# Optimization experiments

Hardware: AMD Instinct MI355X
Metric: run time of the kernel (lower is better)

Reference implementation:

```python
import jax, jax.numpy as jnp
from jax import lax
import numpy as np

B, CIN, H, W = 32, 3, 128, 128
HID = 256          # hidden_dim == embedding_dim
K = 512            # num_embeddings
CC = 0.25          # commitment_cost
RR = 16            # SE reduction ratio


def setup_inputs() -> dict:
    key = jax.random.key(0)
    ks = iter(jax.random.split(key, 40))
    def n(shape, s=0.05):
        return jax.random.normal(next(ks), shape, jnp.float32) * s
    inp = {"x": jax.random.normal(next(ks), (B, CIN, H, W), jnp.float32)}
    inp.update(
        ec1_w=n((HID, CIN, 4, 4)), ec1_b=n((HID,)),
        ec2_w=n((HID, HID, 2, 2)), ec2_b=n((HID,)),
        se1_w1=n((HID // RR, HID)), se1_b1=n((HID // RR,)), se1_w2=n((HID, HID // RR)), se1_b2=n((HID,)), sa1_w=n((1, 2, 7, 7)),
        se2_w1=n((HID // RR, HID)), se2_b1=n((HID // RR,)), se2_w2=n((HID, HID // RR)), se2_b2=n((HID,)), sa2_w=n((1, 2, 7, 7)),
        codebook=jax.random.uniform(next(ks), (K, HID), jnp.float32, -1.0 / K, 1.0 / K),
        dt1_w=n((HID, HID, 2, 2)), dt1_b=n((HID,)),
        dt2_w=n((HID, CIN, 4, 4)), dt2_b=n((CIN,)),
        dse_w1=n((HID // RR, HID)), dse_b1=n((HID // RR,)), dse_w2=n((HID, HID // RR)), dse_b2=n((HID,)), dsa_w=n((2, 1, 7, 7)),
    )
    return inp


def conv(x, w, b, stride, pad=0):
    y = lax.conv_general_dilated(x, w, (stride, stride), [(pad, pad), (pad, pad)],
                                 dimension_numbers=('NCHW', 'OIHW', 'NCHW'))
    return y if b is None else y + b[None, :, None, None]


def convt(x, w, b, stride, pad=0):
    # torch ConvTranspose2d(weight [Cin, Cout, kh, kw]) == conv with flipped kernel,
    # lhs dilated by stride, padding k-1-pad
    k = w.shape[2]
    p = k - 1 - pad
    y = lax.conv_general_dilated(x, jnp.flip(w, (2, 3)), (1, 1), [(p, p), (p, p)],
                                 lhs_dilation=(stride, stride),
                                 dimension_numbers=('NCHW', 'IOHW', 'NCHW'))
    return y if b is None else y + b[None, :, None, None]


def se(x, w1, b1, w2, b2):
    s = jnp.mean(x, (2, 3))                                   # [B, C] global avg pool
    g = jax.nn.sigmoid(jax.nn.relu(s @ w1.T + b1) @ w2.T + b2)
    return x * g[:, :, None, None]


def cbam(x, w1, b1, w2, b2, sw, transpose=False):
    out = se(x, w1, b1, w2, b2)
    cat = jnp.concatenate([jnp.mean(out, 1, keepdims=True), jnp.max(out, 1, keepdims=True)], 1)
    s = convt(cat, sw, None, 1, 3) if transpose else conv(cat, sw, None, 1, 3)
    out = out * jax.nn.sigmoid(s)
    return x * out  # note: original CBAM.forward multiplies by x again


def vq(z, cb):
    D = cb.shape[1]
    flat = z.reshape(-1, D)  # faithful to torch reshape(-1, embedding_dim) on NCHW
    # squared euclidean distances (argmin identical to cdist argmin)
    d2 = jnp.sum(flat * flat, 1, keepdims=True) - 2.0 * (flat @ cb.T) + jnp.sum(cb * cb, 1)
    idx = jnp.argmin(d2, 1)
    q = cb[idx].reshape(z.shape)  # == one_hot(idx) @ cb, without materializing one-hot
    e_loss = jnp.mean((lax.stop_gradient(q) - z) ** 2)
    q_loss = jnp.mean((q - lax.stop_gradient(z)) ** 2)
    loss = q_loss + CC * e_loss
    q_st = z + lax.stop_gradient(q - z)
    p = jnp.zeros((cb.shape[0],), z.dtype).at[idx].add(1.0) / flat.shape[0]
    perplexity = jnp.exp(-jnp.sum(p * jnp.log(p + 1e-10)))
    return loss, q_st, perplexity


def reference(x, ec1_w, ec1_b, ec2_w, ec2_b,
              se1_w1, se1_b1, se1_w2, se1_b2, sa1_w,
              se2_w1, se2_b1, se2_w2, se2_b2, sa2_w,
              codebook, dt1_w, dt1_b, dt2_w, dt2_b,
              dse_w1, dse_b1, dse_w2, dse_b2, dsa_w):
    # encoder
    h = cbam(jax.nn.relu(conv(x, ec1_w, ec1_b, 2)), se1_w1, se1_b1, se1_w2, se1_b2, sa1_w)
    z = cbam(jax.nn.relu(conv(h, ec2_w, ec2_b, 1)), se2_w1, se2_b1, se2_w2, se2_b2, sa2_w)
    # vector quantization
    loss, q, perplexity = vq(z, codebook)
    # decoder
    d = cbam(jax.nn.relu(convt(q, dt1_w, dt1_b, 1)), dse_w1, dse_b1, dse_w2, dse_b2, dsa_w, transpose=True)
    x_recon = convt(d, dt2_w, dt2_b, 2)
    return x_recon, loss, perplexity
```

## Files before the change

kernel.cpp:

```cpp
#include <hip/hip_runtime.h>
#include <math.h>

#define NB 32
#define HID 256
#define HW1 (63*63)
#define HW2 (62*62)
#define T63 ((size_t)NB*HID*HW1)
#define T62 ((size_t)NB*HID*HW2)
#define NROWS 123008
#define KCB 512
#define GATHER_BLOCKS 1024

typedef __attribute__((ext_vector_type(8))) short short8;
typedef __attribute__((ext_vector_type(4))) float f32x4;
typedef __attribute__((ext_vector_type(4))) unsigned short us4;

__device__ __forceinline__ unsigned short f2bf(float f) {
    union { float f; unsigned int u; } v; v.f = f;
    unsigned int u = v.u;
    return (unsigned short)((u + 0x7FFFu + ((u >> 16) & 1u)) >> 16);
}
__device__ __forceinline__ float bf2f(unsigned short u) {
    union { unsigned int i; float f; } v; v.i = ((unsigned int)u) << 16;
    return v.f;
}

__global__ __launch_bounds__(256) void zero_small(float* __restrict__ sse, int* __restrict__ counts) {
    if (threadIdx.x == 0) sse[0] = 0.f;
    for (int i = threadIdx.x; i < KCB; i += 256) counts[i] = 0;
}
__global__ __launch_bounds__(256) void zero_pooled(float* __restrict__ pooled) {
    pooled[blockIdx.x*256 + threadIdx.x] = 0.f;
}

__global__ __launch_bounds__(256) void prepack_c1(
    const float* __restrict__ w, unsigned short* __restrict__ pack) {
    int t = blockIdx.x*256 + threadIdx.x;
    if (t >= 16384) return;
    int j = t & 7, lk = (t >> 3) & 3, co = (t >> 5) & 255, kc = t >> 13;
    int k = kc*32 + lk*8 + j;
    pack[t] = (k < 48) ? f2bf(w[co*48 + k]) : (unsigned short)0;
}

__global__ __launch_bounds__(256) void conv1_mfma(
    const float* __restrict__ x, const unsigned short* __restrict__ apack,
    const float* __restrict__ bias, unsigned short* __restrict__ X0) {
    __shared__ float xs[3][18][18];
    __shared__ __align__(16) unsigned short Bm[64*72];
    int b = blockIdx.y, t = blockIdx.x;
    int oh0 = (t >> 3)*8, ow0 = (t & 7)*8;
    int ih0 = oh0*2, iw0 = ow0*2;
    const float* xb = x + (size_t)b*3*128*128;
    for (int i = threadIdx.x; i < 972; i += 256) {
        int c = i / 324, rem = i - c*324, r = rem / 18, cl = rem - r*18;
        int ih = ih0 + r, iw = iw0 + cl;
        xs[c][r][cl] = (ih < 128 && iw < 128) ? xb[((size_t)c*128 + ih)*128 + iw] : 0.f;
    }
    __syncthreads();
    for (int i = threadIdx.x; i < 2048; i += 256) {
        int px = i >> 5, kp = (i & 31)*2;
        int ph = px >> 3, pw = px & 7;
        unsigned int pk = 0;
        #pragma unroll
        for (int u = 0; u < 2; ++u) {
            int k = kp + u;
            float v = 0.f;
            if (k < 48) {
                int c = k >> 4, k2 = k & 15, kh = k2 >> 2, kw = k2 & 3;
                v = xs[c][ph*2+kh][pw*2+kw];
            }
            pk |= ((unsigned int)f2bf(v)) << (16*u);
        }
        *(unsigned int*)&Bm[px*72 + kp] = pk;
    }
    __syncthreads();

    int w = threadIdx.x >> 6, l = threadIdx.x & 63;
    int lr = l & 15, lk = l >> 4;
    f32x4 acc[4][4];
    #pragma unroll
    for (int i = 0; i < 4; ++i)
        #pragma unroll
        for (int j = 0; j < 4; ++j) acc[i][j] = (f32x4){0.f,0.f,0.f,0.f};

    #pragma unroll
    for (int kc = 0; kc < 2; ++kc) {
        short8 bf[4];
        #pragma unroll
        for (int pxf = 0; pxf < 4; ++pxf)
            bf[pxf] = *(const short8*)&Bm[(pxf*16+lr)*72 + kc*32 + lk*8];
        #pragma unroll
        for (int cof = 0; cof < 4; ++cof) {
            int co = w*64 + cof*16 + lr;
            short8 af = *(const short8*)(apack + (((size_t)kc*256 + co)*4 + (size_t)lk)*8);
            acc[cof][0] = __builtin_amdgcn_mfma_f32_16x16x32_bf16(af, bf[0], acc[cof][0], 0, 0, 0);
            acc[cof][1] = __builtin_amdgcn_mfma_f32_16x16x32_bf16(af, bf[1], acc[cof][1], 0, 0, 0);
            acc[cof][2] = __builtin_amdgcn_mfma_f32_16x16x32_bf16(af, bf[2], acc[cof][2], 0, 0, 0);
            acc[cof][3] = __builtin_amdgcn_mfma_f32_16x16x32_bf16(af, bf[3], acc[cof][3], 0, 0, 0);
        }
    }
    #pragma unroll
    for (int cof = 0; cof < 4; ++cof) {
        int cob = w*64 + cof*16 + lk*4;
        float4 bz = *(const float4*)&bias[cob];
        #pragma unroll
        for (int pxf = 0; pxf < 4; ++pxf) {
            int px = pxf*16 + lr;
            int oh = oh0 + (px >> 3), ow = ow0 + (px & 7);
            if (oh < 63 && ow < 63) {
                f32x4 a = acc[cof][pxf];
                us4 pk = { f2bf(fmaxf(a.x + bz.x, 0.f)), f2bf(fmaxf(a.y + bz.y, 0.f)),
                           f2bf(fmaxf(a.z + bz.z, 0.f)), f2bf(fmaxf(a.w + bz.w, 0.f)) };
                *(us4*)(X0 + ((size_t)b*HW1 + (size_t)oh*63 + ow)*256 + cob) = pk;
            }
        }
    }
}

__global__ __launch_bounds__(256) void gap_nhwc(
    const unsigned short* __restrict__ X, float* __restrict__ pooled,
    int HW, float inv) {
    int b = blockIdx.y;
    int px0 = blockIdx.x * 512;
    int o = threadIdx.x & 31, pg = threadIdx.x >> 5;
    const unsigned short* xb = X + (size_t)b*HW*256 + o*8;
    float acc[8];
    #pragma unroll
    for (int j = 0; j < 8; ++j) acc[j] = 0.f;
    for (int i = 0; i < 64; ++i) {
        int px = px0 + pg + i*8;
        if (px < HW) {
            short8 v = *(const short8*)(xb + (size_t)px*256);
            #pragma unroll
            for (int j = 0; j < 8; ++j) acc[j] += bf2f((unsigned short)v[j]);
        }
    }
    __shared__ float pool2[8][256];
    #pragma unroll
    for (int j = 0; j < 8; ++j) pool2[pg][o*8+j] = acc[j];
    __syncthreads();
    float s = 0.f;
    #pragma unroll
    for (int p = 0; p < 8; ++p) s += pool2[p][threadIdx.x];
    atomicAdd(pooled + b*256 + threadIdx.x, s * inv);
}

__global__ __launch_bounds__(256) void gap_z(
    const unsigned short* __restrict__ Z, float* __restrict__ pooled, int HW) {
    int bc = blockIdx.x;
    const unsigned int* p = (const unsigned int*)(Z + (size_t)bc*HW);
    int n2 = HW >> 1;
    float s = 0.f;
    for (int i = threadIdx.x; i < n2; i += 256) {
        unsigned int v = p[i];
        s += bf2f((unsigned short)(v & 0xffff)) + bf2f((unsigned short)(v >> 16));
    }
    __shared__ float lds[4];
    for (int off = 32; off; off >>= 1) s += __shfl_down(s, off, 64);
    if ((threadIdx.x & 63) == 0) lds[threadIdx.x >> 6] = s;
    __syncthreads();
    if (threadIdx.x == 0) pooled[bc] = (lds[0]+lds[1]+lds[2]+lds[3]) / (float)HW;
}

__global__ __launch_bounds__(256) void se_mlp(
    const float* __restrict__ pooled, const float* __restrict__ w1,
    const float* __restrict__ b1, const float* __restrict__ w2,
    const float* __restrict__ b2, float* __restrict__ g) {
    int b = blockIdx.x;
    __shared__ float ps[256], hs[16];
    ps[threadIdx.x] = pooled[b*256 + threadIdx.x];
    __syncthreads();
    if (threadIdx.x < 16) {
        float a = b1[threadIdx.x];
        const float* wr = w1 + threadIdx.x*256;
        for (int k = 0; k < 256; ++k) a = fmaf(ps[k], wr[k], a);
        hs[threadIdx.x] = fmaxf(a, 0.f);
    }
    __syncthreads();
    float a = b2[threadIdx.x];
    const float* wr = w2 + threadIdx.x*16;
    #pragma unroll
    for (int j = 0; j < 16; ++j) a = fmaf(hs[j], wr[j], a);
    g[b*256 + threadIdx.x] = 1.f / (1.f + expf(-a));
}

__global__ __launch_bounds__(256) void chanpool_nhwc(
    const unsigned short* __restrict__ X, const float* __restrict__ g,
    float* __restrict__ am, int HW) {
    int b = blockIdx.y;
    __shared__ float gs[256];
    gs[threadIdx.x] = g[b*256 + threadIdx.x];
    __syncthreads();
    int p = blockIdx.x*256 + threadIdx.x;
    if (p >= HW) return;
    const unsigned short* xp = X + ((size_t)b*HW + p)*256;
    float s = 0.f, mx = -3.0e38f;
    for (int o = 0; o < 32; ++o) {
        short8 v = *(const short8*)(xp + o*8);
        #pragma unroll
        for (int j = 0; j < 8; ++j) {
            float f = bf2f((unsigned short)v[j]) * gs[o*8+j];
            s += f; mx = fmaxf(mx, f);
        }
    }
    am[((size_t)b*2)*HW + p]   = s * (1.f/256.f);
    am[((size_t)b*2+1)*HW + p] = mx;
}

__global__ __launch_bounds__(256) void chanpool_z(
    const unsigned short* __restrict__ Z, const float* __restrict__ g,
    float* __restrict__ am, int HW) {
    int b = blockIdx.y;
    __shared__ float gs[256];
    gs[threadIdx.x] = g[b*256 + threadIdx.x];
    __syncthreads();
    int p = blockIdx.x*256 + threadIdx.x;
    if (p >= HW) return;
    const unsigned short* xb = Z + (size_t)b*256*HW + p;
    float s = 0.f, mx = -3.0e38f;
    for (int c = 0; c < 256; ++c) {
        float v = bf2f(xb[(size_t)c*HW]) * gs[c];
        s += v; mx = fmaxf(mx, v);
    }
    am[((size_t)b*2)*HW + p]   = s * (1.f/256.f);
    am[((size_t)b*2+1)*HW + p] = mx;
}

__global__ __launch_bounds__(256) void spatial_conv(
    const float* __restrict__ am, const float* __restrict__ sw,
    float* __restrict__ ss, int H, int W, int transpose) {
    int b = blockIdx.y;
    int p = blockIdx.x*256 + threadIdx.x;
    __shared__ float ws[98];
    if (threadIdx.x < 98) {
        int c = threadIdx.x / 49, k = threadIdx.x % 49;
        int kh = k / 7, kw = k % 7;
        ws[threadIdx.x] = transpose ? sw[c*49 + (6-kh)*7 + (6-kw)]
                                    : sw[c*49 + kh*7 + kw];
    }
    __syncthreads();
    if (p >= H*W) return;
    int oh = p / W, ow = p % W;
    float acc = 0.f;
    #pragma unroll
    for (int c = 0; c < 2; ++c) {
        const float* ab = am + ((size_t)b*2 + c)*H*W;
        for (int kh = 0; kh < 7; ++kh) {
            int ih = oh + kh - 3;
            if (ih < 0 || ih >= H) continue;
            for (int kw = 0; kw < 7; ++kw) {
                int iw = ow + kw - 3;
                if (iw < 0 || iw >= W) continue;
                acc = fmaf(ab[(size_t)ih*W + iw], ws[c*49 + kh*7 + kw], acc);
            }
        }
    }
    ss[(size_t)b*H*W + p] = 1.f / (1.f + expf(-acc));
}

__global__ __launch_bounds__(256) void cbam_z(
    unsigned short* Z, const float* __restrict__ g,
    const float* __restrict__ ss, int HW) {
    int b = blockIdx.y;
    int e2 = blockIdx.x*256 + threadIdx.x;
    if (e2 >= 128*HW) return;
    size_t e = (size_t)e2*2;
    int c = (int)(e / HW), p = (int)(e % HW);
    float gc = g[b*256 + c];
    float s0 = ss[(size_t)b*HW + p];
    float s1 = ss[(size_t)b*HW + p + 1];
    unsigned int* px = (unsigned int*)(Z + (size_t)b*256*HW + e);
    unsigned int v = *px;
    float f0 = bf2f((unsigned short)(v & 0xffff));
    float f1 = bf2f((unsigned short)(v >> 16));
    f0 = f0*f0*gc*s0;
    f1 = f1*f1*gc*s1;
    *px = (unsigned int)f2bf(f0) | ((unsigned int)f2bf(f1) << 16);
}

__global__ __launch_bounds__(256) void to_nhwc_bf16(
    const unsigned short* __restrict__ Z, unsigned short* __restrict__ X, int HW) {
    int b = blockIdx.y;
    int p = blockIdx.x*256 + threadIdx.x;
    bool valid = p < HW;
    const unsigned short* inb = Z + (size_t)b*256*HW + p;
    unsigned short* dst = X + ((size_t)b*HW + p)*256;
    #pragma unroll
    for (int ch = 0; ch < 4; ++ch) {
        unsigned short buf[64];
        #pragma unroll
        for (int j = 0; j < 64; ++j)
            buf[j] = valid ? inb[(size_t)(ch*64 + j)*HW] : (unsigned short)0;
        if (valid) {
            #pragma unroll
            for (int j2 = 0; j2 < 8; ++j2)
                *(short8*)(dst + ch*64 + j2*8) = *(const short8*)&buf[j2*8];
        }
    }
}

__global__ __launch_bounds__(256) void prepack_w(
    const float* __restrict__ w, unsigned short* __restrict__ pack, int transpose_flip) {
    int t = blockIdx.x*256 + threadIdx.x;
    int j = t & 7, koct = (t >> 3) & 3, co = (t >> 5) & 255, tap = (t >> 13) & 3, cc = t >> 15;
    int ci = cc*32 + koct*8 + j;
    int kh = tap >> 1, kw = tap & 1;
    float v;
    if (transpose_flip) v = w[((size_t)ci*256 + co)*4 + (1-kh)*2 + (1-kw)];
    else                v = w[((size_t)co*256 + ci)*4 + kh*2 + kw];
    pack[t] = f2bf(v);
}

__global__ __launch_bounds__(256) void prepack_dt2b(
    const float* __restrict__ w, unsigned short* __restrict__ pk) {
    int t = blockIdx.x*256 + threadIdx.x;
    int jj = t & 7, lk = (t >> 3) & 3, co = (t >> 5) & 15, j = (t >> 9) & 3, cc = (t >> 11) & 7, p = t >> 14;
    int ci = cc*32 + lk*8 + jj;
    int kh0 = p >> 1, kw0 = p & 1;
    const int dj[4] = {0, 2, 8, 10};
    float v = 0.f;
    if (co < 3) v = w[(size_t)ci*48 + co*16 + kh0*4 + kw0 + dj[j]];
    pk[t] = f2bf(v);
}

template <int MODE>
__global__ __launch_bounds__(256) void convk2_mfma_nhwc(
    const unsigned short* __restrict__ Xin, const unsigned short* __restrict__ apack,
    const float* __restrict__ bias, const float* __restrict__ gvec,
    const float* __restrict__ ssm, unsigned short* __restrict__ outZ,
    unsigned short* __restrict__ outU,
    int inH, int inW, int outH, int outW, int pad) {
    __shared__ __align__(16) unsigned short Sh[MODE ? 16896 : 13600];
    __shared__ float gs[256];
    unsigned short* Ir0 = Sh;
    unsigned short* Ir1 = Sh + 6800;
    int b = blockIdx.y;
    int raw = blockIdx.x;
    int xcd = raw & 7, jj = raw >> 3;
    int t = (xcd + 8*(jj >> 2))*4 + (jj & 3);
    int oh0 = (t >> 2) * 4, ow0 = (t & 3) * 16;
    int w = threadIdx.x >> 6, l = threadIdx.x & 63;
    int lr = l & 15, lk = l >> 4;
    const unsigned short* src = Xin + (size_t)b*inH*inW*256;
    const float* ssb = (MODE == 0) ? (ssm + (size_t)b*inH*inW) : (const float*)0;
    if (MODE == 0) {
        gs[threadIdx.x] = gvec[b*256 + threadIdx.x];
        __syncthreads();
    }

    f32x4 acc[4][4];
    #pragma unroll
    for (int i = 0; i < 4; ++i)
        #pragma unroll
        for (int j = 0; j < 4; ++j) acc[i][j] = (f32x4){0.f,0.f,0.f,0.f};

    auto STAGE = [&](int cc, int bufi) {
        unsigned short* Ib = bufi ? Ir1 : Ir0;
        #pragma unroll
        for (int pass = 0; pass < 3; ++pass) {
            int u = pass*256 + threadIdx.x;
            if (u < 680) {
                int sub = (u >= 340) ? 1 : 0;
                int uu = u - sub*340;
                int sp = uu >> 2, q = uu & 3;
                int r = (sp*241) >> 12, c = sp - r*17;
                int gh = oh0 + r - pad, gw = ow0 + c - pad;
                short8 v = (short8){0,0,0,0,0,0,0,0};
                bool valid = (gh >= 0) && (gh < inH) && (gw >= 0) && (gw < inW);
                if (valid)
                    v = *(const short8*)(src + ((size_t)gh*inW + gw)*256 + (cc+sub)*32 + q*8);
                if (MODE == 0) {
                    if (valid) {
                        float sv = ssb[(size_t)gh*inW + gw];
                        int c0 = (cc+sub)*32 + q*8;
                        unsigned int pk[4];
                        #pragma unroll
                        for (int j = 0; j < 4; ++j) {
                            float f0 = bf2f((unsigned short)v[2*j]);
                            float f1 = bf2f((unsigned short)v[2*j+1]);
                            f0 = f0*f0*gs[c0+2*j]*sv;
                            f1 = f1*f1*gs[c0+2*j+1]*sv;
                            pk[j] = (unsigned int)f2bf(f0) | ((unsigned int)f2bf(f1) << 16);
                        }
                        v = *(const short8*)pk;
                    }
                }
                *(short8*)&Ib[sub*3400 + sp*40 + q*8] = v;
            }
        }
    };

    STAGE(0, 0);
    for (int cc = 0; cc < 8; cc += 2) {
        __syncthreads();
        if (cc < 6) STAGE(cc+2, ((cc >> 1) + 1) & 1);
        const unsigned short* Ibase = ((cc >> 1) & 1) ? Ir1 : Ir0;
        #pragma unroll
        for (int half = 0; half < 2; ++half) {
            const unsigned short* Ib = Ibase + half*3400;
            #pragma unroll
            for (int tap = 0; tap < 4; ++tap) {
                int kh = tap >> 1, kw = tap & 1;
                int spb = kh*17 + kw + lr;
                short8 b0 = *(const short8*)&Ib[(spb     )*40 + lk*8];
                short8 b1 = *(const short8*)&Ib[(spb + 17)*40 + lk*8];
                short8 b2 = *(const short8*)&Ib[(spb + 34)*40 + lk*8];
                short8 b3 = *(const short8*)&Ib[(spb + 51)*40 + lk*8];
                const unsigned short* abase = apack + (((size_t)((cc+half)*4 + tap)*256)*4 + (size_t)lk)*8;
                #pragma unroll
                for (int cof = 0; cof < 4; ++cof) {
                    int co = w*64 + cof*16 + lr;
                    short8 af = *(const short8*)(abase + (size_t)co*32);
                    acc[cof][0] = __builtin_amdgcn_mfma_f32_16x16x32_bf16(af, b0, acc[cof][0], 0, 0, 0);
                    acc[cof][1] = __builtin_amdgcn_mfma_f32_16x16x32_bf16(af, b1, acc[cof][1], 0, 0, 0);
                    acc[cof][2] = __builtin_amdgcn_mfma_f32_16x16x32_bf16(af, b2, acc[cof][2], 0, 0, 0);
                    acc[cof][3] = __builtin_amdgcn_mfma_f32_16x16x32_bf16(af, b3, acc[cof][3], 0, 0, 0);
                }
            }
        }
    }
    if (MODE == 0) {
        int ow = ow0 + lr;
        #pragma unroll
        for (int cof = 0; cof < 4; ++cof) {
            int cob = w*64 + cof*16 + lk*4;
            float4 bz = *(const float4*)&bias[cob];
            #pragma unroll
            for (int pxf = 0; pxf < 4; ++pxf) {
                int oh = oh0 + pxf;
                if (oh < outH && ow < outW) {
                    f32x4 a = acc[cof][pxf];
                    size_t base = ((size_t)(b*256 + cob)*outH + oh)*outW + ow;
                    size_t st = (size_t)outH*outW;
                    outZ[base]        = f2bf(fmaxf(a.x + bz.x, 0.f));
                    outZ[base +   st] = f2bf(fmaxf(a.y + bz.y, 0.f));
                    outZ[base + 2*st] = f2bf(fmaxf(a.z + bz.z, 0.f));
                    outZ[base + 3*st] = f2bf(fmaxf(a.w + bz.w, 0.f));
                }
            }
        }
    } else {
        __syncthreads();
        #pragma unroll
        for (int cof = 0; cof < 4; ++cof) {
            int cob = w*64 + cof*16 + lk*4;
            float4 bz = *(const float4*)&bias[cob];
            #pragma unroll
            for (int pxf = 0; pxf < 4; ++pxf) {
                f32x4 a = acc[cof][pxf];
                us4 pk = { f2bf(fmaxf(a.x + bz.x, 0.f)), f2bf(fmaxf(a.y + bz.y, 0.f)),
                           f2bf(fmaxf(a.z + bz.z, 0.f)), f2bf(fmaxf(a.w + bz.w, 0.f)) };
                *(us4*)&Sh[(pxf*16 + lr)*264 + cob] = pk;
            }
        }
        __syncthreads();
        int owp = threadIdx.x >> 4, c0 = (threadIdx.x & 15)*16;
        int ow = ow0 + owp;
        #pragma unroll
        for (int row = 0; row < 4; ++row) {
            int oh = oh0 + row;
            if (oh < outH && ow < outW) {
                unsigned short* dst = outU + (((size_t)b*outH + oh)*outW + ow)*256 + c0;
                *(short8*)dst       = *(const short8*)&Sh[(row*16 + owp)*264 + c0];
                *(short8*)(dst + 8) = *(const short8*)&Sh[(row*16 + owp)*264 + c0 + 8];
            }
        }
    }
}

__global__ __launch_bounds__(256) void cb_norm(
    const float* __restrict__ cb, float* __restrict__ cbn) {
    for (int n = threadIdx.x; n < KCB; n += 256) {
        float s = 0.f;
        for (int k = 0; k < 256; ++k) { float v = cb[(size_t)n*256+k]; s = fmaf(v,v,s); }
        cbn[n] = s;
    }
}

__global__ __launch_bounds__(256) void cb_pack(
    const float* __restrict__ cb, unsigned short* __restrict__ cbp) {
    int t = blockIdx.x*256 + threadIdx.x;
    cbp[t] = f2bf(cb[t]);
}

__global__ __launch_bounds__(256) void vq_assign_mfma(
    const unsigned short* __restrict__ z, const unsigned short* __restrict__ cbp,
    const float* __restrict__ cbn, int* __restrict__ idx) {
    __shared__ __align__(16) unsigned short zb[64*264];
    __shared__ __align__(16) unsigned short cbs[2][32*264];
    __shared__ float cbl[KCB];
    int r0 = blockIdx.x * 64;
    for (int v = threadIdx.x; v < 2048; v += 256) {
        int row = v >> 5, o = v & 31;
        *(short8*)&zb[row*264 + o*8] = *(const short8*)&z[(size_t)(r0+row)*256 + o*8];
    }
    for (int i = threadIdx.x; i < KCB; i += 256) cbl[i] = cbn[i];
    int tcode = threadIdx.x >> 3, tk = threadIdx.x & 7;
    auto STAGE_CB = [&](int c, int bufi) {
        const unsigned short* src = cbp + ((size_t)(c*32 + tcode))*256 + tk*8;
        unsigned short* dst = &cbs[bufi][tcode*264 + tk*8];
        #pragma unroll
        for (int j = 0; j < 4; ++j)
            *(short8*)(dst + j*64) = *(const short8*)(src + j*64);
    };
    STAGE_CB(0, 0);
    __syncthreads();

    int w = threadIdx.x >> 6, l = threadIdx.x & 63;
    int lr = l & 15, lk = l >> 4;
    short8 afr[8];
    #pragma unroll
    for (int ks = 0; ks < 8; ++ks)
        afr[ks] = *(const short8*)&zb[(w*16 + lr)*264 + ks*32 + lk*8];

    float bd[4]; int bi[4];
    #pragma unroll
    for (int r = 0; r < 4; ++r) { bd[r] = 3.0e38f; bi[r] = 0; }

    for (int c = 0; c < 16; ++c) {
        if (c < 15) STAGE_CB(c+1, (c+1)&1);
        const unsigned short* Cb = cbs[c & 1];
        #pragma unroll
        for (int f = 0; f < 2; ++f) {
            f32x4 acc = (f32x4){0.f,0.f,0.f,0.f};
            #pragma unroll
            for (int ks = 0; ks < 8; ++ks) {
                short8 bfr = *(const short8*)&Cb[(f*16 + lr)*264 + ks*32 + lk*8];
                acc = __builtin_amdgcn_mfma_f32_16x16x32_bf16(afr[ks], bfr, acc, 0, 0, 0);
            }
            int n = c*32 + f*16 + lr;
            float cn = cbl[n];
            #pragma unroll
            for (int r = 0; r < 4; ++r) {
                float dist = fmaf(-2.f, acc[r], cn);
                if (dist < bd[r]) { bd[r] = dist; bi[r] = n; }
            }
        }
        __syncthreads();
    }
    #pragma unroll
    for (int r = 0; r < 4; ++r) {
        #pragma unroll
        for (int off = 1; off < 16; off <<= 1) {
            float od = __shfl_xor(bd[r], off, 64);
            int   oi = __shfl_xor(bi[r], off, 64);
            if (od < bd[r] || (od == bd[r] && oi < bi[r])) { bd[r] = od; bi[r] = oi; }
        }
    }
    if (lr == 0) {
        #pragma unroll
        for (int r = 0; r < 4; ++r)
            idx[r0 + w*16 + lk*4 + r] = bi[r];
    }
}

__global__ __launch_bounds__(256) void vq_gather(
    unsigned short* zq, const float* __restrict__ cb,
    const int* __restrict__ idx, float* __restrict__ sse, int* __restrict__ counts) {
    __shared__ int hist[KCB];
    for (int i = threadIdx.x; i < KCB; i += 256) hist[i] = 0;
    __syncthreads();
    float local = 0.f;
    for (int r = blockIdx.x; r < NROWS; r += GATHER_BLOCKS) {
        int id = idx[r];
        if (threadIdx.x == 0) atomicAdd(&hist[id], 1);
        float qv = cb[(size_t)id*256 + threadIdx.x];
        unsigned short* pz = zq + (size_t)r*256 + threadIdx.x;
        float zv = bf2f(*pz);
        *pz = f2bf(qv);
        float d = qv - zv;
        local = fmaf(d, d, local);
    }
    __shared__ float lds[4];
    for (int off = 32; off; off >>= 1) local += __shfl_down(local, off, 64);
    if ((threadIdx.x & 63) == 0) lds[threadIdx.x >> 6] = local;
    __syncthreads();
    if (threadIdx.x == 0) atomicAdd(sse, lds[0]+lds[1]+lds[2]+lds[3]);
    for (int i = threadIdx.x; i < KCB; i += 256) {
        int h = hist[i];
        if (h) atomicAdd(counts + i, h);
    }
}

__global__ __launch_bounds__(256) void vq_finalize(
    const float* __restrict__ sse, const int* __restrict__ counts,
    float* __restrict__ out) {
    __shared__ float lds[4];
    float h = 0.f;
    for (int n = threadIdx.x; n < KCB; n += 256) {
        float p = (float)counts[n] * (1.f/123008.f);
        h += p * logf(p + 1e-10f);
    }
    for (int off = 32; off; off >>= 1) h += __shfl_down(h, off, 64);
    if ((threadIdx.x & 63) == 0) lds[threadIdx.x >> 6] = h;
    __syncthreads();
    if (threadIdx.x == 0) {
        out[1572864] = 1.25f * sse[0] / 31490048.f;
        out[1572865] = expf(-(lds[0]+lds[1]+lds[2]+lds[3]));
    }
}

__global__ __launch_bounds__(256) void dt2_mfma(
    const unsigned short* __restrict__ Y, const unsigned short* __restrict__ apack,
    const float* __restrict__ bias, const float* __restrict__ gvec,
    const float* __restrict__ ssm, float* __restrict__ out) {
    __shared__ __align__(16) unsigned short Iraw[2][289*40];
    __shared__ float gs[256];
    int b = blockIdx.y, t = blockIdx.x;
    int a0 = (t >> 2)*16, b0 = (t & 3)*16;
    int p = threadIdx.x >> 6;
    int l = threadIdx.x & 63;
    int lr = l & 15, lk = l >> 4;
    const unsigned short* src = Y + (size_t)b*HW1*256;
    const float* ssb = ssm + (size_t)b*HW1;
    gs[threadIdx.x] = gvec[b*256 + threadIdx.x];
    __syncthreads();

    auto STAGE = [&](int cc, int bufi) {
        #pragma unroll
        for (int pass = 0; pass < 5; ++pass) {
            int u = pass*256 + threadIdx.x;
            if (u < 1156) {
                int sp = u >> 2, q = u & 3;
                int r = (sp*241) >> 12, c = sp - r*17;
                int ia = a0 - 1 + r, ib = b0 - 1 + c;
                short8 v = (short8){0,0,0,0,0,0,0,0};
                bool valid = (ia >= 0) && (ia < 63) && (ib >= 0) && (ib < 63);
                if (valid) {
                    v = *(const short8*)(src + ((size_t)ia*63 + ib)*256 + cc*32 + q*8);
                    float sv = ssb[(size_t)ia*63 + ib];
                    int c0 = cc*32 + q*8;
                    unsigned int pk[4];
                    #pragma unroll
                    for (int j = 0; j < 4; ++j) {
                        float f0 = bf2f((unsigned short)v[2*j]);
                        float f1 = bf2f((unsigned short)v[2*j+1]);
                        f0 = f0*f0*gs[c0+2*j]*sv;
                        f1 = f1*f1*gs[c0+2*j+1]*sv;
                        pk[j] = (unsigned int)f2bf(f0) | ((unsigned int)f2bf(f1) << 16);
                    }
                    v = *(const short8*)pk;
                }
                *(short8*)&Iraw[bufi][sp*40 + q*8] = v;
            }
        }
    };

    f32x4 acc[16];
    #pragma unroll
    for (int i = 0; i < 16; ++i) acc[i] = (f32x4){0.f,0.f,0.f,0.f};

    STAGE(0, 0);
    for (int cc = 0; cc < 8; ++cc) {
        __syncthreads();
        if (cc < 7) STAGE(cc+1, (cc+1)&1);
        const unsigned short* Ib = Iraw[cc & 1];
        #pragma unroll
        for (int j = 0; j < 4; ++j) {
            int jh = j >> 1, jw = j & 1;
            short8 af = *(const short8*)(apack +
                ((size_t)((p*8 + cc)*4 + j))*512 + lr*32 + lk*8);
            int sp0 = (1 - jh)*17 + (lr + 1 - jw);
            #pragma unroll
            for (int nf = 0; nf < 16; ++nf) {
                short8 bf = *(const short8*)&Ib[(sp0 + nf*17)*40 + lk*8];
                acc[nf] = __builtin_amdgcn_mfma_f32_16x16x32_bf16(af, bf, acc[nf], 0, 0, 0);
            }
        }
    }
    if (lk == 0) {
        int kh0 = p >> 1, kw0 = p & 1;
        float bz0 = bias[0], bz1 = bias[1], bz2 = bias[2];
        int wp = 2*(b0 + lr) + kw0;
        #pragma unroll
        for (int nf = 0; nf < 16; ++nf) {
            int h = 2*(a0 + nf) + kh0;
            size_t ob = (size_t)(b*3)*16384 + (size_t)h*128 + wp;
            out[ob]         = acc[nf].x + bz0;
            out[ob + 16384] = acc[nf].y + bz1;
            out[ob + 32768] = acc[nf].z + bz2;
        }
    }
}

extern "C" void kernel_launch(void* const* d_in, const int* in_sizes, int n_in,
                              void* d_out, int out_size, void* d_ws, size_t ws_size,
                              hipStream_t stream) {
    const float* x      = (const float*)d_in[0];
    const float* ec1_w  = (const float*)d_in[1];
    const float* ec1_b  = (const float*)d_in[2];
    const float* ec2_w  = (const float*)d_in[3];
    const float* ec2_b  = (const float*)d_in[4];
    const float* se1_w1 = (const float*)d_in[5];
    const float* se1_b1 = (const float*)d_in[6];
    const float* se1_w2 = (const float*)d_in[7];
    const float* se1_b2 = (const float*)d_in[8];
    const float* sa1_w  = (const float*)d_in[9];
    const float* se2_w1 = (const float*)d_in[10];
    const float* se2_b1 = (const float*)d_in[11];
    const float* se2_w2 = (const float*)d_in[12];
    const float* se2_b2 = (const float*)d_in[13];
    const float* sa2_w  = (const float*)d_in[14];
    const float* cbk    = (const float*)d_in[15];
    const float* dt1_w  = (const float*)d_in[16];
    const float* dt1_b  = (const float*)d_in[17];
    const float* dt2_w  = (const float*)d_in[18];
    const float* dt2_b  = (const float*)d_in[19];
    const float* dse_w1 = (const float*)d_in[20];
    const float* dse_b1 = (const float*)d_in[21];
    const float* dse_w2 = (const float*)d_in[22];
    const float* dse_b2 = (const float*)d_in[23];
    const float* dsa_w  = (const float*)d_in[24];
    float* out = (float*)d_out;

    unsigned short* Zb = (unsigned short*)d_ws;
    unsigned short* U0 = Zb + T62;
    unsigned short* U1 = U0 + T63;
    float* pooled = (float*)(U1 + T63);
    float* g      = pooled + 8192;
    float* am     = g + 8192;
    float* ssmap  = am + (size_t)NB*2*HW1;
    float* cbn    = ssmap + (size_t)NB*HW1;
    unsigned short* apackE = (unsigned short*)(cbn + 512);
    unsigned short* apackD = apackE + 262144;
    unsigned short* cbp    = apackD + 262144;
    unsigned short* apackC = cbp + 131072;
    unsigned short* apack2 = apackC + 16384;
    float* sse    = (float*)(apack2 + 65536);
    int*   counts = (int*)(sse + 1);
    int*   idx    = counts + 512;

    zero_small<<<1, 256, 0, stream>>>(sse, counts);
    prepack_w<<<1024, 256, 0, stream>>>(ec2_w, apackE, 0);
    prepack_w<<<1024, 256, 0, stream>>>(dt1_w, apackD, 1);
    prepack_c1<<<64, 256, 0, stream>>>(ec1_w, apackC);
    prepack_dt2b<<<256, 256, 0, stream>>>(dt2_w, apack2);
    cb_norm<<<1, 256, 0, stream>>>(cbk, cbn);
    cb_pack<<<512, 256, 0, stream>>>(cbk, cbp);

    conv1_mfma<<<dim3(64, NB), 256, 0, stream>>>(x, apackC, ec1_b, U0);
    zero_pooled<<<32, 256, 0, stream>>>(pooled);
    gap_nhwc<<<dim3(8, NB), 256, 0, stream>>>(U0, pooled, HW1, 1.f/HW1);
    se_mlp<<<NB, 256, 0, stream>>>(pooled, se1_w1, se1_b1, se1_w2, se1_b2, g);
    chanpool_nhwc<<<dim3(16, NB), 256, 0, stream>>>(U0, g, am, HW1);
    spatial_conv<<<dim3(16, NB), 256, 0, stream>>>(am, sa1_w, ssmap, 63, 63, 0);

    convk2_mfma_nhwc<0><<<dim3(64, NB), 256, 0, stream>>>(U0, apackE, ec2_b, g, ssmap, Zb, (unsigned short*)0, 63, 63, 62, 62, 0);
    gap_z<<<NB*256, 256, 0, stream>>>(Zb, pooled, HW2);
    se_mlp<<<NB, 256, 0, stream>>>(pooled, se2_w1, se2_b1, se2_w2, se2_b2, g);
    chanpool_z<<<dim3(16, NB), 256, 0, stream>>>(Zb, g, am, HW2);
    spatial_conv<<<dim3(16, NB), 256, 0, stream>>>(am, sa2_w, ssmap, 62, 62, 0);
    cbam_z<<<dim3(1922, NB), 256, 0, stream>>>(Zb, g, ssmap, HW2);

    vq_assign_mfma<<<NROWS/64, 256, 0, stream>>>(Zb, cbp, cbn, idx);
    vq_gather<<<GATHER_BLOCKS, 256, 0, stream>>>(Zb, cbk, idx, sse, counts);
    vq_finalize<<<1, 256, 0, stream>>>(sse, counts, out);
    to_nhwc_bf16<<<dim3(16, NB), 256, 0, stream>>>(Zb, U1, HW2);

    convk2_mfma_nhwc<1><<<dim3(64, NB), 256, 0, stream>>>(U1, apackD, dt1_b, (const float*)0, (const float*)0, (unsigned short*)0, U0, 62, 62, 63, 63, 1);
    zero_pooled<<<32, 256, 0, stream>>>(pooled);
    gap_nhwc<<<dim3(8, NB), 256, 0, stream>>>(U0, pooled, HW1, 1.f/HW1);
    se_mlp<<<NB, 256, 0, stream>>>(pooled, dse_w1, dse_b1, dse_w2, dse_b2, g);
    chanpool_nhwc<<<dim3(16, NB), 256, 0, stream>>>(U0, g, am, HW1);
    spatial_conv<<<dim3(16, NB), 256, 0, stream>>>(am, dsa_w, ssmap, 63, 63, 1);

    dt2_mfma<<<dim3(16, NB), 256, 0, stream>>>(U0, apack2, dt2_b, g, ssmap, out);
}
```

Baseline: 722.8 us.

## Fuse VQ gather into assignment and gather codebook directly in NHWC transpose

Removes the separate vq_gather kernel. The assignment kernel now computes the squared error as ||z||^2 plus the best distance, and accumulates the histogram in LDS before flushing it to global counts. The NHWC transpose kernel now reads codebook rows through idx instead of the quantized Zb buffer, which saves a full read-modify-write pass over Zb. In exchange, the transpose performs indirect idx and codebook loads per element, and the loss now comes from the bf16 distance expansion rather than a direct difference.

```diff
diff --git a/kernel.cpp b/kernel.cpp
--- a/kernel.cpp
+++ b/kernel.cpp
@@ -9,7 +9,6 @@
 #define T62 ((size_t)NB*HID*HW2)
 #define NROWS 123008
 #define KCB 512
-#define GATHER_BLOCKS 1024
 
 typedef __attribute__((ext_vector_type(8))) short short8;
 typedef __attribute__((ext_vector_type(4))) float f32x4;
@@ -278,19 +277,25 @@
     *px = (unsigned int)f2bf(f0) | ((unsigned int)f2bf(f1) << 16);
 }
 
-__global__ __launch_bounds__(256) void to_nhwc_bf16(
-    const unsigned short* __restrict__ Z, unsigned short* __restrict__ X, int HW) {
+__global__ __launch_bounds__(256) void to_nhwc_gather(
+    const float* __restrict__ cb, const int* __restrict__ idx,
+    unsigned short* __restrict__ X, int HW) {
     int b = blockIdx.y;
     int p = blockIdx.x*256 + threadIdx.x;
     bool valid = p < HW;
-    const unsigned short* inb = Z + (size_t)b*256*HW + p;
-    unsigned short* dst = X + ((size_t)b*HW + p)*256;
+    int pp = valid ? p : 0;
+    size_t flatBase = (size_t)b*256*HW + pp;
+    unsigned short* dst = X + ((size_t)b*HW + pp)*256;
     #pragma unroll
     for (int ch = 0; ch < 4; ++ch) {
         unsigned short buf[64];
         #pragma unroll
-        for (int j = 0; j < 64; ++j)
-            buf[j] = valid ? inb[(size_t)(ch*64 + j)*HW] : (unsigned short)0;
+        for (int j = 0; j < 64; ++j) {
+            size_t flat = flatBase + (size_t)(ch*64 + j)*HW;
+            int row = (int)(flat >> 8);
+            int k   = (int)(flat & 255);
+            buf[j] = f2bf(cb[(size_t)idx[row]*256 + k]);
+        }
         if (valid) {
             #pragma unroll
             for (int j2 = 0; j2 < 8; ++j2)
@@ -485,16 +490,21 @@
 
 __global__ __launch_bounds__(256) void vq_assign_mfma(
     const unsigned short* __restrict__ z, const unsigned short* __restrict__ cbp,
-    const float* __restrict__ cbn, int* __restrict__ idx) {
+    const float* __restrict__ cbn, int* __restrict__ idx,
+    float* __restrict__ sse, int* __restrict__ counts) {
     __shared__ __align__(16) unsigned short zb[64*264];
     __shared__ __align__(16) unsigned short cbs[2][32*264];
     __shared__ float cbl[KCB];
+    __shared__ float znp[64][4];
+    __shared__ int   hist[KCB];
+    __shared__ float ssel;
     int r0 = blockIdx.x * 64;
     for (int v = threadIdx.x; v < 2048; v += 256) {
         int row = v >> 5, o = v & 31;
         *(short8*)&zb[row*264 + o*8] = *(const short8*)&z[(size_t)(r0+row)*256 + o*8];
     }
-    for (int i = threadIdx.x; i < KCB; i += 256) cbl[i] = cbn[i];
+    for (int i = threadIdx.x; i < KCB; i += 256) { cbl[i] = cbn[i]; hist[i] = 0; }
+    if (threadIdx.x == 0) ssel = 0.f;
     int tcode = threadIdx.x >> 3, tk = threadIdx.x & 7;
     auto STAGE_CB = [&](int c, int bufi) {
         const unsigned short* src = cbp + ((size_t)(c*32 + tcode))*256 + tk*8;
@@ -506,6 +516,21 @@
     STAGE_CB(0, 0);
     __syncthreads();
 
+    {
+        int rowz = threadIdx.x >> 2, qz = threadIdx.x & 3;
+        float s = 0.f;
+        #pragma unroll
+        for (int j = 0; j < 8; ++j) {
+            short8 v = *(const short8*)&zb[rowz*264 + qz*64 + j*8];
+            #pragma unroll
+            for (int e = 0; e < 8; ++e) {
+                float f = bf2f((unsigned short)v[e]);
+                s = fmaf(f, f, s);
+            }
+        }
+        znp[rowz][qz] = s;
+    }
+
     int w = threadIdx.x >> 6, l = threadIdx.x & 63;
     int lr = l & 15, lk = l >> 4;
     short8 afr[8];
@@ -548,34 +573,19 @@
         }
     }
     if (lr == 0) {
-        #pragma unroll
-        for (int r = 0; r < 4; ++r)
-            idx[r0 + w*16 + lk*4 + r] = bi[r];
-    }
-}
-
-__global__ __launch_bounds__(256) void vq_gather(
-    unsigned short* zq, const float* __restrict__ cb,
-    const int* __restrict__ idx, float* __restrict__ sse, int* __restrict__ counts) {
-    __shared__ int hist[KCB];
-    for (int i = threadIdx.x; i < KCB; i += 256) hist[i] = 0;
-    __syncthreads();
-    float local = 0.f;
-    for (int r = blockIdx.x; r < NROWS; r += GATHER_BLOCKS) {
-        int id = idx[r];
-        if (threadIdx.x == 0) atomicAdd(&hist[id], 1);
-        float qv = cb[(size_t)id*256 + threadIdx.x];
-        unsigned short* pz = zq + (size_t)r*256 + threadIdx.x;
-        float zv = bf2f(*pz);
-        *pz = f2bf(qv);
-        float d = qv - zv;
-        local = fmaf(d, d, local);
-    }
-    __shared__ float lds[4];
-    for (int off = 32; off; off >>= 1) local += __shfl_down(local, off, 64);
-    if ((threadIdx.x & 63) == 0) lds[threadIdx.x >> 6] = local;
-    __syncthreads();
-    if (threadIdx.x == 0) atomicAdd(sse, lds[0]+lds[1]+lds[2]+lds[3]);
+        float local = 0.f;
+        #pragma unroll
+        for (int r = 0; r < 4; ++r) {
+            int row = w*16 + lk*4 + r;
+            idx[r0 + row] = bi[r];
+            float zn = znp[row][0] + znp[row][1] + znp[row][2] + znp[row][3];
+            local += zn + bd[r];
+            atomicAdd(&hist[bi[r]], 1);
+        }
+        atomicAdd(&ssel, local);
+    }
+    __syncthreads();
+    if (threadIdx.x == 0) atomicAdd(sse, ssel);
     for (int i = threadIdx.x; i < KCB; i += 256) {
         int h = hist[i];
         if (h) atomicAdd(counts + i, h);
@@ -752,10 +762,9 @@
     spatial_conv<<<dim3(16, NB), 256, 0, stream>>>(am, sa2_w, ssmap, 62, 62, 0);
     cbam_z<<<dim3(1922, NB), 256, 0, stream>>>(Zb, g, ssmap, HW2);
 
-    vq_assign_mfma<<<NROWS/64, 256, 0, stream>>>(Zb, cbp, cbn, idx);
-    vq_gather<<<GATHER_BLOCKS, 256, 0, stream>>>(Zb, cbk, idx, sse, counts);
+    vq_assign_mfma<<<NROWS/64, 256, 0, stream>>>(Zb, cbp, cbn, idx, sse, counts);
     vq_finalize<<<1, 256, 0, stream>>>(sse, counts, out);
-    to_nhwc_bf16<<<dim3(16, NB), 256, 0, stream>>>(Zb, U1, HW2);
+    to_nhwc_gather<<<dim3(16, NB), 256, 0, stream>>>(cbk, idx, U1, HW2);
 
     convk2_mfma_nhwc<1><<<dim3(64, NB), 256, 0, stream>>>(U1, apackD, dt1_b, (const float*)0, (const float*)0, (unsigned short*)0, U0, 62, 62, 63, 63, 1);
     zero_pooled<<<32, 256, 0, stream>>>(pooled);
```

Result: no change. 732.9 us (+1.4%).
